# Kernel optimization log

Measured on AMD Instinct MI355X. Metric: run time of the kernel, lower is better.

## Reference

```python
import jax, jax.numpy as jnp
import numpy as np

NOISE_EPS = 0.01
LB_COEFF = 0.01
TOP_K = 2


def setup_inputs() -> dict:
    key = jax.random.key(0)
    k1, k2, k3 = jax.random.split(key, 3)
    B, S, H, E = 4, 4096, 4096, 8
    x = jax.random.normal(k1, (B, S, H), dtype=jnp.float32)
    W = jax.random.normal(k2, (H, E), dtype=jnp.float32) * (1.0 / np.sqrt(H))
    b = jnp.zeros((E,), dtype=jnp.float32)
    noise = jax.random.normal(k3, (B * S, E), dtype=jnp.float32)
    return {"x": x, "W": W, "b": b, "noise": noise}


def reference(x, W, b, noise):
    B, S, H = x.shape
    E = W.shape[1]
    x_flat = x.reshape(-1, H)                      # [BS, H]
    logits = x_flat @ W + b + noise * NOISE_EPS    # [BS, E]
    routing_weights = jax.nn.softmax(logits, axis=-1)
    top_k_weights, top_k_indices = jax.lax.top_k(routing_weights, TOP_K)
    top_k_weights = top_k_weights / jnp.sum(top_k_weights, axis=-1, keepdims=True)
    # load-balancing aux loss
    expert_usage = jnp.mean(routing_weights, axis=0)        # [E]
    target = 1.0 / E
    aux_loss = LB_COEFF * jnp.sum((expert_usage - target) ** 2)
    return (top_k_weights.reshape(B, S, TOP_K),
            top_k_indices.reshape(B, S, TOP_K),
            aux_loss)
```

## Files before the change

kernel.cpp:

```cpp
#include <hip/hip_runtime.h>


#define BS      16384
#define HDIM    4096
#define NE      8
#define RPW     4
#define WPB     4
#define NOISE_EPS 0.01f
#define LB_COEFF  0.01f

__global__ __launch_bounds__(256, 4)
void router_main(const float* __restrict__ x, const float* __restrict__ W,
                 const float* __restrict__ bias, const float* __restrict__ noise,
                 float* __restrict__ out, float* __restrict__ usage_ws) {
    const int tid  = threadIdx.x;
    const int lane = tid & 63;
    const int wave = tid >> 6;
    const int group = blockIdx.x * WPB + wave;
    const int row0  = group * RPW;

    __shared__ float block_usage[NE];
    if (tid < NE) block_usage[tid] = 0.0f;
    __syncthreads();

    float acc[RPW][NE];
#pragma unroll
    for (int r = 0; r < RPW; ++r)
#pragma unroll
        for (int e = 0; e < NE; ++e) acc[r][e] = 0.0f;

    const float4* __restrict__ W4 = (const float4*)W;
    const float4* __restrict__ x4 = (const float4*)(x + (size_t)row0 * HDIM);

    for (int it = 0; it < (HDIM / 4 / 64); ++it) {
        const int f = it * 64 + lane;

        float4 xr[RPW];
#pragma unroll
        for (int r = 0; r < RPW; ++r)
            xr[r] = x4[(size_t)r * (HDIM / 4) + f];

        float4 w[8];
#pragma unroll
        for (int j = 0; j < 8; ++j) w[j] = W4[(size_t)f * 8 + j];

#pragma unroll
        for (int r = 0; r < RPW; ++r) {
#pragma unroll
            for (int k = 0; k < 4; ++k) {
                const float xv = (k == 0) ? xr[r].x : (k == 1) ? xr[r].y
                               : (k == 2) ? xr[r].z : xr[r].w;
                const float4 wlo = w[2 * k], whi = w[2 * k + 1];
                acc[r][0] += xv * wlo.x; acc[r][1] += xv * wlo.y;
                acc[r][2] += xv * wlo.z; acc[r][3] += xv * wlo.w;
                acc[r][4] += xv * whi.x; acc[r][5] += xv * whi.y;
                acc[r][6] += xv * whi.z; acc[r][7] += xv * whi.w;
            }
        }
    }

#pragma unroll
    for (int r = 0; r < RPW; ++r)
#pragma unroll
        for (int e = 0; e < NE; ++e) {
            float v = acc[r][e];
#pragma unroll
            for (int m = 1; m < 64; m <<= 1) v += __shfl_xor(v, m, 64);
            acc[r][e] = v;
        }

    if (lane < RPW) {
        const int row = row0 + lane;

        float logits[NE];
#pragma unroll
        for (int r = 0; r < RPW; ++r)
            if (lane == r)
#pragma unroll
                for (int e = 0; e < NE; ++e) logits[e] = acc[r][e];

        const float4 b_lo = ((const float4*)bias)[0];
        const float4 b_hi = ((const float4*)bias)[1];
        const float4 n_lo = ((const float4*)(noise + (size_t)row * NE))[0];
        const float4 n_hi = ((const float4*)(noise + (size_t)row * NE))[1];

        logits[0] += b_lo.x + NOISE_EPS * n_lo.x;
        logits[1] += b_lo.y + NOISE_EPS * n_lo.y;
        logits[2] += b_lo.z + NOISE_EPS * n_lo.z;
        logits[3] += b_lo.w + NOISE_EPS * n_lo.w;
        logits[4] += b_hi.x + NOISE_EPS * n_hi.x;
        logits[5] += b_hi.y + NOISE_EPS * n_hi.y;
        logits[6] += b_hi.z + NOISE_EPS * n_hi.z;
        logits[7] += b_hi.w + NOISE_EPS * n_hi.w;

        float m = logits[0];
#pragma unroll
        for (int e = 1; e < NE; ++e) m = fmaxf(m, logits[e]);
        float p[NE], s = 0.0f;
#pragma unroll
        for (int e = 0; e < NE; ++e) { p[e] = expf(logits[e] - m); s += p[e]; }
        const float inv_s = 1.0f / s;

        float v1 = p[0]; int e1 = 0;
#pragma unroll
        for (int e = 1; e < NE; ++e) if (p[e] > v1) { v1 = p[e]; e1 = e; }
        float v2 = -1.0f; int e2 = 0;
#pragma unroll
        for (int e = 0; e < NE; ++e)
            if (e != e1 && p[e] > v2) { v2 = p[e]; e2 = e; }

        const float inv_d = 1.0f / (v1 + v2);
        out[(size_t)row * 2]     = v1 * inv_d;
        out[(size_t)row * 2 + 1] = v2 * inv_d;
        out[(size_t)(BS * 2) + row * 2]     = (float)e1;
        out[(size_t)(BS * 2) + row * 2 + 1] = (float)e2;

#pragma unroll
        for (int e = 0; e < NE; ++e)
            atomicAdd(&block_usage[e], p[e] * inv_s);
    }

    __syncthreads();
    if (tid < NE) atomicAdd(usage_ws + tid, block_usage[tid]);
}

__global__ void router_finalize(const float* __restrict__ usage_ws,
                                float* __restrict__ out) {
    if (threadIdx.x == 0) {
        float aux = 0.0f;
#pragma unroll
        for (int e = 0; e < NE; ++e) {
            const float mean = usage_ws[e] * (1.0f / (float)BS);
            const float d = mean - (1.0f / (float)NE);
            aux += d * d;
        }
        out[(size_t)BS * 4] = LB_COEFF * aux;
    }
}

extern "C" void kernel_launch(void* const* d_in, const int* in_sizes, int n_in,
                              void* d_out, int out_size, void* d_ws, size_t ws_size,
                              hipStream_t stream) {
    const float* x     = (const float*)d_in[0];
    const float* W     = (const float*)d_in[1];
    const float* b     = (const float*)d_in[2];
    const float* noise = (const float*)d_in[3];
    float* out = (float*)d_out;
    float* usage = (float*)d_ws;

    hipMemsetAsync(usage, 0, NE * sizeof(float), stream);

    const int groups = BS / RPW;
    const int blocks = groups / WPB;
    router_main<<<blocks, 256, 0, stream>>>(x, W, b, noise, out, usage);
    router_finalize<<<1, 64, 0, stream>>>(usage, out);
}
```

Baseline: 415.0 us.

## Stage W in swizzled LDS and double-buffer x loads with 1024-thread blocks

```diff
diff --git a/kernel.cpp b/kernel.cpp
--- a/kernel.cpp
+++ b/kernel.cpp
@@ -5,22 +5,31 @@
 #define HDIM    4096
 #define NE      8
 #define RPW     4
-#define WPB     4
+#define NWAVE   16
+#define NITER   (HDIM / 4 / 64)
 #define NOISE_EPS 0.01f
 #define LB_COEFF  0.01f
 
-__global__ __launch_bounds__(256, 4)
+__global__ __launch_bounds__(1024, 4)
 void router_main(const float* __restrict__ x, const float* __restrict__ W,
                  const float* __restrict__ bias, const float* __restrict__ noise,
                  float* __restrict__ out, float* __restrict__ usage_ws) {
     const int tid  = threadIdx.x;
     const int lane = tid & 63;
     const int wave = tid >> 6;
-    const int group = blockIdx.x * WPB + wave;
-    const int row0  = group * RPW;
+    const int row0 = blockIdx.x * (NWAVE * RPW) + wave * RPW;
 
+    __shared__ float4 w_lds[HDIM * 2];
     __shared__ float block_usage[NE];
     if (tid < NE) block_usage[tid] = 0.0f;
+    {
+        const float4* __restrict__ W4 = (const float4*)W;
+#pragma unroll
+        for (int i = tid; i < HDIM * 2; i += 1024) {
+            const int f = i >> 3, j = i & 7;
+            w_lds[(i & ~7) | (j ^ (f & 7))] = W4[i];
+        }
+    }
     __syncthreads();
 
     float acc[RPW][NE];
@@ -29,35 +38,60 @@
 #pragma unroll
         for (int e = 0; e < NE; ++e) acc[r][e] = 0.0f;
 
-    const float4* __restrict__ W4 = (const float4*)W;
     const float4* __restrict__ x4 = (const float4*)(x + (size_t)row0 * HDIM);
+    const int wxor = lane & 7;
 
-    for (int it = 0; it < (HDIM / 4 / 64); ++it) {
-        const int f = it * 64 + lane;
+    float4 xa[RPW], xb[RPW];
+#pragma unroll
+    for (int r = 0; r < RPW; ++r)
+        xa[r] = x4[(size_t)r * (HDIM / 4) + lane];
 
-        float4 xr[RPW];
+#define FMA_HALF(XC, F, KK)                                                   \
+    {                                                                         \
+        float4 wr[4];                                                         \
+        _Pragma("unroll")                                                     \
+        for (int m = 0; m < 4; ++m)                                           \
+            wr[m] = w_lds[(F) * 8 + ((4 * (KK) + m) ^ wxor)];                 \
+        _Pragma("unroll")                                                     \
+        for (int r = 0; r < RPW; ++r) {                                       \
+            _Pragma("unroll")                                                 \
+            for (int kq = 0; kq < 2; ++kq) {                                  \
+                const int k = 2 * (KK) + kq;                                  \
+                const float xv = ((const float*)&XC[r])[k];                   \
+                acc[r][0] += xv * wr[2 * kq].x;                               \
+                acc[r][1] += xv * wr[2 * kq].y;                               \
+                acc[r][2] += xv * wr[2 * kq].z;                               \
+                acc[r][3] += xv * wr[2 * kq].w;                               \
+                acc[r][4] += xv * wr[2 * kq + 1].x;                           \
+                acc[r][5] += xv * wr[2 * kq + 1].y;                           \
+                acc[r][6] += xv * wr[2 * kq + 1].z;                           \
+                acc[r][7] += xv * wr[2 * kq + 1].w;                           \
+            }                                                                 \
+        }                                                                     \
+    }
+
+#pragma unroll 1
+    for (int it = 0; it < NITER; it += 2) {
+        {
+            const int fn = (it + 1) * 64 + lane;
 #pragma unroll
-        for (int r = 0; r < RPW; ++r)
-            xr[r] = x4[(size_t)r * (HDIM / 4) + f];
-
-        float4 w[8];
+            for (int r = 0; r < RPW; ++r)
+                xb[r] = x4[(size_t)r * (HDIM / 4) + fn];
+            const int f = it * 64 + lane;
+            FMA_HALF(xa, f, 0)
+            FMA_HALF(xa, f, 1)
+        }
+        {
+            const int fn = ((it + 2 < NITER) ? (it + 2) : (NITER - 1)) * 64 + lane;
 #pragma unroll
-        for (int j = 0; j < 8; ++j) w[j] = W4[(size_t)f * 8 + j];
-
-#pragma unroll
-        for (int r = 0; r < RPW; ++r) {
-#pragma unroll
-            for (int k = 0; k < 4; ++k) {
-                const float xv = (k == 0) ? xr[r].x : (k == 1) ? xr[r].y
-                               : (k == 2) ? xr[r].z : xr[r].w;
-                const float4 wlo = w[2 * k], whi = w[2 * k + 1];
-                acc[r][0] += xv * wlo.x; acc[r][1] += xv * wlo.y;
-                acc[r][2] += xv * wlo.z; acc[r][3] += xv * wlo.w;
-                acc[r][4] += xv * whi.x; acc[r][5] += xv * whi.y;
-                acc[r][6] += xv * whi.z; acc[r][7] += xv * whi.w;
-            }
+            for (int r = 0; r < RPW; ++r)
+                xa[r] = x4[(size_t)r * (HDIM / 4) + fn];
+            const int f = (it + 1) * 64 + lane;
+            FMA_HALF(xb, f, 0)
+            FMA_HALF(xb, f, 1)
         }
     }
+#undef FMA_HALF
 
 #pragma unroll
     for (int r = 0; r < RPW; ++r)
@@ -150,8 +184,7 @@
 
     hipMemsetAsync(usage, 0, NE * sizeof(float), stream);
 
-    const int groups = BS / RPW;
-    const int blocks = groups / WPB;
-    router_main<<<blocks, 256, 0, stream>>>(x, W, b, noise, out, usage);
+    const int blocks = BS / (NWAVE * RPW);
+    router_main<<<blocks, 1024, 0, stream>>>(x, W, b, noise, out, usage);
     router_finalize<<<1, 64, 0, stream>>>(usage, out);
 }
```

Measured after the change: 371.5 us. 1.12x faster.
